# Kernel optimization log

Measured on AMD Instinct MI355X. Metric: run time of the kernel, lower is better.

## Reference

```python
import jax, jax.numpy as jnp
import numpy as np


def _unfold_valid(x, kh, kw, stride):
    """torch.nn.Unfold equivalent (valid padding): [B,C,H,W] -> [B, C*kh*kw, L].
    Channel-major patch layout (c, kh, kw), matching PyTorch."""
    B, C, H, W = x.shape
    oh = (H - kh) // stride + 1
    ow = (W - kw) // stride + 1
    i = (jnp.arange(oh) * stride)[:, None] + jnp.arange(kh)  # [oh, kh]
    j = (jnp.arange(ow) * stride)[:, None] + jnp.arange(kw)  # [ow, kw]
    # advanced indexing broadcasts to [B, C, oh, ow, kh, kw]
    p = x[:, :, i[:, None, :, None], j[None, :, None, :]]
    p = p.transpose(0, 1, 4, 5, 2, 3).reshape(B, C * kh * kw, oh * ow)
    return p


def setup_inputs() -> dict:
    root = jax.random.key(0)
    k1, k2 = jax.random.split(root)
    query = jax.random.normal(k1, (4, 32, 64, 64), dtype=jnp.float32)
    key = jax.random.normal(k2, (4, 32, 64, 192), dtype=jnp.float32)
    return {"query": query, "key": key}


def reference(query, key):
    stride = 1
    B, C, Hq, Wq = query.shape
    P = key.shape[3] - Wq + 1
    patches = _unfold_valid(key, Hq, Wq, stride)          # [B, D, L], D = C*Hq*Wq
    q = query.reshape(B, C * Hq * Wq, 1)                  # [B, D, 1]
    y = jnp.mean(jnp.abs(patches - q), axis=1)            # [B, L] L1 cost volume
    relevance_maps = jnp.min(y, axis=1, keepdims=True)    # [B, 1]
    hard_indices = jnp.argmin(y, axis=1).reshape(-1)      # [B]
    return hard_indices, P, relevance_maps
```

## Files before the change

kernel.cpp:

```cpp
#include <hip/hip_runtime.h>
#include <math.h>

#define B 4
#define C 32
#define H 64
#define WQ 64
#define WK 192
#define NP 129
#define ROWS (C * H)
#define ELEMS (ROWS * WQ)
#define GB 256
#define WPB 4
#define RPW 2
#define PSTRIDE 132
#define KPAD 200

__global__ __launch_bounds__(256, 4) void patch_l1_partial(const float* __restrict__ query,
                                                           const float* __restrict__ key,
                                                           float* __restrict__ part) {
    __shared__ __align__(16) float kbuf[WPB][RPW][KPAD];
    __shared__ float red[WPB][130];

    const int bid  = blockIdx.x;
    const int b    = bid >> 8;
    const int g    = bid & (GB - 1);
    const int t    = threadIdx.x;
    const int wv   = t >> 6;
    const int lane = t & 63;
    const int slot = __builtin_amdgcn_readfirstlane(g * WPB + (t >> 6));
    const int r0   = slot * RPW;

    const float* __restrict__ qb = query + (size_t)b * ELEMS;
    const float* __restrict__ kb = key   + (size_t)b * ROWS * WK + (size_t)r0 * WK;

    if (lane < 48) {
        const float4 v0 = *reinterpret_cast<const float4*>(kb + lane * 4);
        const float4 v1 = *reinterpret_cast<const float4*>(kb + WK + lane * 4);
        *reinterpret_cast<float4*>(&kbuf[wv][0][lane * 4]) = v0;
        *reinterpret_cast<float4*>(&kbuf[wv][1][lane * 4]) = v1;
    }
    const float q0l = qb[(size_t)r0 * WQ + lane];
    const float q1l = qb[(size_t)(r0 + 1) * WQ + lane];

    float acc_a = 0.f, acc_b = 0.f, acc2 = 0.f;

    #pragma unroll
    for (int rr = 0; rr < RPW; ++rr) {
        const float* __restrict__ qr = qb + (size_t)(r0 + rr) * WQ;
        float qs[64];
        #pragma unroll
        for (int s4 = 0; s4 < 16; ++s4) {
            const float4 qv = *reinterpret_cast<const float4*>(qr + s4 * 4);
            qs[s4 * 4 + 0] = qv.x; qs[s4 * 4 + 1] = qv.y;
            qs[s4 * 4 + 2] = qv.z; qs[s4 * 4 + 3] = qv.w;
        }

        const float* __restrict__ k0 = &kbuf[wv][rr][0];
        float aa0 = 0.f, aa1 = 0.f, bb0 = 0.f, bb1 = 0.f;

        #pragma unroll
        for (int si = 0; si < 16; ++si) {
            const int s = si * 4;
            const float2 ka = *reinterpret_cast<const float2*>(&k0[2 * lane + s]);
            const float2 kc = *reinterpret_cast<const float2*>(&k0[2 * lane + s + 2]);
            aa0 += fabsf(ka.x - qs[s]);
            if (si > 0) bb0 += fabsf(ka.x - qs[s - 1]);
            aa1 += fabsf(ka.y - qs[s + 1]);
            bb1 += fabsf(ka.y - qs[s]);
            aa0 += fabsf(kc.x - qs[s + 2]);
            bb0 += fabsf(kc.x - qs[s + 1]);
            aa1 += fabsf(kc.y - qs[s + 3]);
            bb1 += fabsf(kc.y - qs[s + 2]);
        }
        bb0 += fabsf(k0[2 * lane + 64] - qs[63]);

        acc_a += aa0 + aa1;
        acc_b += bb0 + bb1;
        acc2  += fabsf(k0[128 + lane] - (rr ? q1l : q0l));
    }

    #pragma unroll
    for (int m = 32; m; m >>= 1) acc2 += __shfl_xor(acc2, m, 64);

    *reinterpret_cast<float2*>(&red[wv][2 * lane]) = make_float2(acc_a, acc_b);
    if (lane == 0) red[wv][128] = acc2;
    __syncthreads();

    if (t < NP)
        part[(size_t)bid * PSTRIDE + t] = red[0][t] + red[1][t] + red[2][t] + red[3][t];
}

__global__ __launch_bounds__(1024) void patch_l1_final(const float* __restrict__ part,
                                                       float* __restrict__ out) {
    const int b    = blockIdx.x;
    const int t    = threadIdx.x;
    const int wv   = t >> 6;
    const int lane = t & 63;

    float acc0 = 0.f, acc1 = 0.f, acc2 = 0.f;
    #pragma unroll 4
    for (int g = wv; g < GB; g += 16) {
        const float* __restrict__ src = part + ((size_t)b * GB + g) * PSTRIDE;
        acc0 += src[lane];
        acc1 += src[64 + lane];
        if (lane == 0) acc2 += src[128];
    }

    __shared__ float red[16][NP];
    red[wv][lane]      = acc0;
    red[wv][64 + lane] = acc1;
    if (lane == 0) red[wv][128] = acc2;
    __syncthreads();

    float y = INFINITY;
    int idx = NP;
    if (t < NP) {
        float s = 0.f;
        #pragma unroll
        for (int w = 0; w < 16; ++w) s += red[w][t];
        y = s * (1.0f / (float)ELEMS);
        idx = t;
    }

    __shared__ float sy[256];
    __shared__ int   si[256];
    if (t < 256) { sy[t] = y; si[t] = idx; }
    __syncthreads();
    #pragma unroll
    for (int s = 128; s > 0; s >>= 1) {
        if (t < s) {
            const float yo = sy[t + s];
            const int   io = si[t + s];
            if (yo < sy[t] || (yo == sy[t] && io < si[t])) {
                sy[t] = yo;
                si[t] = io;
            }
        }
        __syncthreads();
    }

    if (t == 0) {
        out[b]     = (float)si[0];
        out[5 + b] = sy[0];
        if (b == 0) out[4] = (float)NP;
    }
}

extern "C" void kernel_launch(void* const* d_in, const int* in_sizes, int n_in,
                              void* d_out, int out_size, void* d_ws, size_t ws_size,
                              hipStream_t stream) {
    const float* query = (const float*)d_in[0];
    const float* key   = (const float*)d_in[1];
    float* out  = (float*)d_out;
    float* part = (float*)d_ws;

    patch_l1_partial<<<B * GB, 256, 0, stream>>>(query, key, part);
    patch_l1_final<<<B, 1024, 0, stream>>>(part, out);
}
```

Before: 19.37 us.

## Use larger partial blocks and transpose partials for wave-reduced final argmin

The partial kernel now runs 16 waves per block over 64 blocks per batch instead of 4 waves over 256, so each block pre-reduces more rows and writes four times fewer partial sums. Partials are stored transposed as [b][p][g], so the final kernel lets each wave read 64 contiguous partials per position, reduce them with shuffles and track its own running min. The shared-memory tree reduction is replaced by a short serial compare across 8 waves. In exchange, the 1024-thread blocks and the larger shared buffers may lower occupancy and scheduling flexibility in the main kernel.

```diff
diff --git a/kernel.cpp b/kernel.cpp
--- a/kernel.cpp
+++ b/kernel.cpp
@@ -9,20 +9,19 @@
 #define NP 129
 #define ROWS (C * H)
 #define ELEMS (ROWS * WQ)
-#define GB 256
-#define WPB 4
+#define GB 64
+#define WPB 16
 #define RPW 2
-#define PSTRIDE 132
 #define KPAD 200
 
-__global__ __launch_bounds__(256, 4) void patch_l1_partial(const float* __restrict__ query,
-                                                           const float* __restrict__ key,
-                                                           float* __restrict__ part) {
+__global__ __launch_bounds__(1024, 4) void patch_l1_partial(const float* __restrict__ query,
+                                                            const float* __restrict__ key,
+                                                            float* __restrict__ part) {
     __shared__ __align__(16) float kbuf[WPB][RPW][KPAD];
     __shared__ float red[WPB][130];
 
     const int bid  = blockIdx.x;
-    const int b    = bid >> 8;
+    const int b    = bid >> 6;
     const int g    = bid & (GB - 1);
     const int t    = threadIdx.x;
     const int wv   = t >> 6;
@@ -86,62 +85,48 @@
     if (lane == 0) red[wv][128] = acc2;
     __syncthreads();
 
-    if (t < NP)
-        part[(size_t)bid * PSTRIDE + t] = red[0][t] + red[1][t] + red[2][t] + red[3][t];
+    if (t < NP) {
+        float s = 0.f;
+        #pragma unroll
+        for (int w = 0; w < WPB; ++w) s += red[w][t];
+        part[((size_t)b * NP + t) * GB + g] = s;
+    }
 }
 
-__global__ __launch_bounds__(1024) void patch_l1_final(const float* __restrict__ part,
-                                                       float* __restrict__ out) {
+__global__ __launch_bounds__(512) void patch_l1_final(const float* __restrict__ part,
+                                                      float* __restrict__ out) {
     const int b    = blockIdx.x;
     const int t    = threadIdx.x;
     const int wv   = t >> 6;
     const int lane = t & 63;
 
-    float acc0 = 0.f, acc1 = 0.f, acc2 = 0.f;
-    #pragma unroll 4
-    for (int g = wv; g < GB; g += 16) {
-        const float* __restrict__ src = part + ((size_t)b * GB + g) * PSTRIDE;
-        acc0 += src[lane];
-        acc1 += src[64 + lane];
-        if (lane == 0) acc2 += src[128];
+    float best  = INFINITY;
+    int   besti = NP;
+
+    for (int p = wv; p < NP; p += 8) {
+        float v = part[((size_t)b * NP + p) * GB + lane];
+        #pragma unroll
+        for (int m = 32; m; m >>= 1) v += __shfl_xor(v, m, 64);
+        const float y = v * (1.0f / (float)ELEMS);
+        if (y < best) { best = y; besti = p; }
     }
 
-    __shared__ float red[16][NP];
-    red[wv][lane]      = acc0;
-    red[wv][64 + lane] = acc1;
-    if (lane == 0) red[wv][128] = acc2;
+    __shared__ float sy[8];
+    __shared__ int   si[8];
+    if (lane == 0) { sy[wv] = best; si[wv] = besti; }
     __syncthreads();
 
-    float y = INFINITY;
-    int idx = NP;
-    if (t < NP) {
-        float s = 0.f;
+    if (t == 0) {
+        float yb = sy[0];
+        int   ib = si[0];
         #pragma unroll
-        for (int w = 0; w < 16; ++w) s += red[w][t];
-        y = s * (1.0f / (float)ELEMS);
-        idx = t;
-    }
-
-    __shared__ float sy[256];
-    __shared__ int   si[256];
-    if (t < 256) { sy[t] = y; si[t] = idx; }
-    __syncthreads();
-    #pragma unroll
-    for (int s = 128; s > 0; s >>= 1) {
-        if (t < s) {
-            const float yo = sy[t + s];
-            const int   io = si[t + s];
-            if (yo < sy[t] || (yo == sy[t] && io < si[t])) {
-                sy[t] = yo;
-                si[t] = io;
-            }
+        for (int w = 1; w < 8; ++w) {
+            const float yo = sy[w];
+            const int   io = si[w];
+            if (yo < yb || (yo == yb && io < ib)) { yb = yo; ib = io; }
         }
-        __syncthreads();
-    }
-
-    if (t == 0) {
-        out[b]     = (float)si[0];
-        out[5 + b] = sy[0];
+        out[b]     = (float)ib;
+        out[5 + b] = yb;
         if (b == 0) out[4] = (float)NP;
     }
 }
@@ -154,6 +139,6 @@
     float* out  = (float*)d_out;
     float* part = (float*)d_ws;
 
-    patch_l1_partial<<<B * GB, 256, 0, stream>>>(query, key, part);
-    patch_l1_final<<<B, 1024, 0, stream>>>(part, out);
+    patch_l1_partial<<<B * GB, 1024, 0, stream>>>(query, key, part);
+    patch_l1_final<<<B, 512, 0, stream>>>(part, out);
 }
```

Result: slower. 20.93 us (+8.1%).

## Transpose partial-sum layout so final reduction reads contiguous float4 per position

Applied to the files above, without the earlier changes.

The partial kernel now writes its per-block sums position-major ([b][position][group]) instead of group-major with padding. The final kernel gives each position 8 threads that read contiguous float4s and combine them with shuffles, replacing the strided 16-wave accumulation and the 16-row shared reduction. The goal is shorter latency and fewer shared-memory passes in the tail kernel. The partial kernel's stores become strided across groups and are no longer coalesced.

```diff
diff --git a/kernel.cpp b/kernel.cpp
--- a/kernel.cpp
+++ b/kernel.cpp
@@ -12,7 +12,6 @@
 #define GB 256
 #define WPB 4
 #define RPW 2
-#define PSTRIDE 132
 #define KPAD 200
 
 __global__ __launch_bounds__(256, 4) void patch_l1_partial(const float* __restrict__ query,
@@ -86,45 +85,55 @@
     if (lane == 0) red[wv][128] = acc2;
     __syncthreads();
 
-    if (t < NP)
-        part[(size_t)bid * PSTRIDE + t] = red[0][t] + red[1][t] + red[2][t] + red[3][t];
+    if (t < NP) {
+        const float v = red[0][t] + red[1][t] + red[2][t] + red[3][t];
+        part[((size_t)b * NP + t) * GB + g] = v;
+    }
 }
 
 __global__ __launch_bounds__(1024) void patch_l1_final(const float* __restrict__ part,
                                                        float* __restrict__ out) {
-    const int b    = blockIdx.x;
-    const int t    = threadIdx.x;
-    const int wv   = t >> 6;
-    const int lane = t & 63;
+    const int b   = blockIdx.x;
+    const int t   = threadIdx.x;
+    const int p   = t >> 3;
+    const int sub = t & 7;
 
-    float acc0 = 0.f, acc1 = 0.f, acc2 = 0.f;
-    #pragma unroll 4
-    for (int g = wv; g < GB; g += 16) {
-        const float* __restrict__ src = part + ((size_t)b * GB + g) * PSTRIDE;
-        acc0 += src[lane];
-        acc1 += src[64 + lane];
-        if (lane == 0) acc2 += src[128];
+    const float inv = 1.0f / (float)ELEMS;
+
+    const float* __restrict__ src = part + ((size_t)b * NP + p) * GB + sub * 32;
+    float4 s4 = make_float4(0.f, 0.f, 0.f, 0.f);
+    #pragma unroll
+    for (int j = 0; j < 8; ++j) {
+        const float4 v = *reinterpret_cast<const float4*>(src + j * 4);
+        s4.x += v.x; s4.y += v.y; s4.z += v.z; s4.w += v.w;
+    }
+    float v = (s4.x + s4.y) + (s4.z + s4.w);
+    v += __shfl_xor(v, 1, 64);
+    v += __shfl_xor(v, 2, 64);
+    v += __shfl_xor(v, 4, 64);
+
+    float v128 = 0.f;
+    if (t < 64) {
+        const float4 w4 = *reinterpret_cast<const float4*>(part + ((size_t)b * NP + 128) * GB + t * 4);
+        v128 = (w4.x + w4.y) + (w4.z + w4.w);
+        #pragma unroll
+        for (int m = 32; m; m >>= 1) v128 += __shfl_xor(v128, m, 64);
     }
 
-    __shared__ float red[16][NP];
-    red[wv][lane]      = acc0;
-    red[wv][64 + lane] = acc1;
-    if (lane == 0) red[wv][128] = acc2;
+    __shared__ float red[NP];
+    if (sub == 0) red[p] = v * inv;
+    if (t == 0)   red[128] = v128 * inv;
     __syncthreads();
-
-    float y = INFINITY;
-    int idx = NP;
-    if (t < NP) {
-        float s = 0.f;
-        #pragma unroll
-        for (int w = 0; w < 16; ++w) s += red[w][t];
-        y = s * (1.0f / (float)ELEMS);
-        idx = t;
-    }
 
     __shared__ float sy[256];
     __shared__ int   si[256];
-    if (t < 256) { sy[t] = y; si[t] = idx; }
+    if (t < 256) {
+        float y = INFINITY;
+        int idx = NP;
+        if (t < NP) { y = red[t]; idx = t; }
+        sy[t] = y;
+        si[t] = idx;
+    }
     __syncthreads();
     #pragma unroll
     for (int s = 128; s > 0; s >>= 1) {
```

Result: faster. 18.60 us (median of 2 runs) (-4.0%).
